# Performance work log

Measured on AMD Instinct MI355X. Metric: run time of the kernel, lower is better.

The kernel has to match this reference:

```python
import jax, jax.numpy as jnp
import numpy as np

B, E, H, DEPTH = 4096, 512, 512, 1
STRIDE = 2 * H * (DEPTH + 1)      # 2048
DEPTH_SIZE = 2 * 4 * H            # 4096


def setup_inputs() -> dict:
    key = jax.random.key(0)
    ks = jax.random.split(key, 12)
    s = 0.02
    return {
        "X": jax.random.normal(ks[0], (B, E), jnp.float32),
        "prev_a": jax.random.normal(ks[1], (B, DEPTH + 1, H), jnp.float32),
        "prev_b": jax.random.normal(ks[2], (B, DEPTH + 1, H), jnp.float32),
        "prev_depth": jax.random.randint(ks[3], (B, 1), 0, DEPTH + 1, jnp.int32),
        "Wa00": jax.random.normal(ks[4], (H, E + 2 * H), jnp.float32) * s,
        "Wa10": jax.random.normal(ks[5], (H, E + H), jnp.float32) * s,
        "Wb00": jax.random.normal(ks[6], (H, E + 2 * H), jnp.float32) * s,
        "Wb11": jax.random.normal(ks[7], (H, E + H), jnp.float32) * s,
        "Wb10": jax.random.normal(ks[8], (H, E + H), jnp.float32) * s,
        "Wb01": jax.random.normal(ks[9], (H, E + 2 * H), jnp.float32) * s,
        "Watt": jax.random.normal(ks[10], (4, DEPTH_SIZE * DEPTH), jnp.float32) * s,
    }


def reference(X, prev_a, prev_b, prev_depth, Wa00, Wa10, Wb00, Wb11, Wb10, Wb01, Watt):
    b = X.shape[0]
    pd = prev_depth.astype(X.dtype)  # [B,1], broadcasts over feature dim
    zeros2h = jnp.zeros((b, 2 * H), X.dtype)
    ab00, ab01, ab10, ab11 = [zeros2h], [zeros2h], [zeros2h], [zeros2h]
    for d in range(1, DEPTH + 1):
        fd = jnp.float32(d)
        a_d, a_dm1 = prev_a[:, d, :], prev_a[:, d - 1, :]
        b_d, b_dm1 = prev_b[:, d, :], prev_b[:, d - 1, :]
        # 'lt' branch multiplies zeros -> drop it; keep eq/gt terms only
        eq0, gt0 = (pd == fd).astype(X.dtype), (pd > fd).astype(X.dtype)
        eqp, gtp = (pd + 1 == fd).astype(X.dtype), (pd + 1 > fd).astype(X.dtype)
        eqm, gtm = (pd - 1 == fd).astype(X.dtype), (pd - 1 > fd).astype(X.dtype)
        fork_join_a = a_d
        nofork_nojoin_a = jnp.concatenate((X, b_dm1, a_d), 1) @ Wa00.T
        fork_nojoin_a = jnp.concatenate((X, b_dm1), 1) @ Wa10.T
        nofork_join_a = a_dm1
        na00 = eq0 * nofork_nojoin_a + gt0 * a_d
        na11 = eq0 * fork_join_a + gt0 * a_d
        na10 = eqp * fork_nojoin_a + gtp * a_d
        na01 = eqm * nofork_join_a + gtm * a_d
        fork_join_b = jnp.concatenate((X, b_d), 1) @ Wb11.T
        nofork_nojoin_b = jnp.concatenate((X, a_d, na00), 1) @ Wb00.T
        fork_nojoin_b = jnp.concatenate((X, na10), 1) @ Wb10.T
        nofork_join_b = jnp.concatenate((X, b_dm1, a_d), 1) @ Wb01.T
        nb00 = eq0 * nofork_nojoin_b + gt0 * b_d
        nb11 = eq0 * fork_join_b + gt0 * b_d
        nb10 = eqp * fork_nojoin_b + gtp * b_d
        nb01 = eqm * nofork_join_b + gtm * b_d
        ab00.append(jnp.concatenate((na00, nb00), 1))
        ab01.append(jnp.concatenate((na01, nb01), 1))
        ab10.append(jnp.concatenate((na10, nb10), 1))
        ab11.append(jnp.concatenate((na11, nb11), 1))
    # each branch: stack over depth+1 -> [B, stride]; concat branches -> [B, 4*stride]
    flats = [jnp.stack(lst, 1).reshape(b, -1) for lst in (ab00, ab01, ab10, ab11)]
    ns = jnp.concatenate(flats, 1)  # [B, 4*STRIDE]
    att = jax.nn.softmax(ns[:, DEPTH_SIZE:] @ Watt.T, axis=-1)  # [B,4]
    e0 = (pd == 0).astype(X.dtype)
    ed = (pd == DEPTH).astype(X.dtype)
    mask = jnp.concatenate((1 - e0, 1 - e0, 1 - ed, 1 - e0), 1)  # [B,4]
    att_vars = mask * att
    # np tiny underflows to 0 in fp32 -> selection is one-hot at the row max
    sel = jnp.sign(att_vars - att_vars.max(1, keepdims=True)) + 1.0
    # striper/stripe_expander bmm == per-row selection of one stride-block
    hidden = jnp.einsum('bc,bcs->bs', sel, ns.reshape(b, 4, STRIDE))
    hidden = hidden.reshape(b, DEPTH + 1, 2 * H)
    next_a = hidden[:, :, :H]
    next_b = hidden[:, :, H:]
    sel_i = sel.astype(prev_depth.dtype)
    pd0 = prev_depth[:, 0]
    next_depth = (sel_i[:, 0] * pd0 + sel_i[:, 1] * (pd0 - 1)
                  + sel_i[:, 2] * (pd0 + 1) + sel_i[:, 3] * pd0)[:, None]
    f = (sel[:, 2] + sel[:, 3])[:, None]
    j = (sel[:, 1] + sel[:, 3])[:, None]
    return next_a, next_b, next_depth, (f, j)
```

## Files before the change

### kernel.cpp

```cpp
#include <hip/hip_runtime.h>
#include <hip/hip_bf16.h>
#include <stdint.h>


typedef __attribute__((ext_vector_type(8))) short bf16x8;
typedef __attribute__((ext_vector_type(4))) float f32x4;

#define MB_ ((size_t)1 << 20)

static __device__ __forceinline__ unsigned short f2bf(float x) {
  unsigned u = __float_as_uint(x);
  return (unsigned short)((u + 0x7FFFu + ((u >> 16) & 1u)) >> 16);
}
static __device__ __forceinline__ float bf2f(unsigned short b) {
  return __uint_as_float((unsigned)b << 16);
}
static __device__ __forceinline__ void cvt8(float4 v0, float4 v1, uint4& hi, uint4& lo) {
  float v[8] = {v0.x, v0.y, v0.z, v0.w, v1.x, v1.y, v1.z, v1.w};
  unsigned hw[4], lw[4];
#pragma unroll
  for (int j = 0; j < 4; ++j) {
    unsigned short h0 = f2bf(v[2 * j]), h1 = f2bf(v[2 * j + 1]);
    unsigned short l0 = f2bf(v[2 * j] - bf2f(h0));
    unsigned short l1 = f2bf(v[2 * j + 1] - bf2f(h1));
    hw[j] = (unsigned)h0 | ((unsigned)h1 << 16);
    lw[j] = (unsigned)l0 | ((unsigned)l1 << 16);
  }
  hi = make_uint4(hw[0], hw[1], hw[2], hw[3]);
  lo = make_uint4(lw[0], lw[1], lw[2], lw[3]);
}

__global__ void kinit(float* nextA, float* nextB, int* cnt, int Bn) {
  long i = (long)blockIdx.x * blockDim.x + threadIdx.x;
  long st = (long)gridDim.x * blockDim.x;
  float4 z = make_float4(0.f, 0.f, 0.f, 0.f);
  long nA = (long)Bn * 128;
  for (long t = i; t < nA; t += st)
    ((float4*)(nextA + (t >> 7) * 1024))[t & 127] = z;
  long nB = (long)Bn * 256;
  for (long t = i; t < nB; t += st) ((float4*)nextB)[t] = z;
  if (blockIdx.x == 0 && threadIdx.x < 16) cnt[threadIdx.x] = 0;
}

struct CvtSeg { const float* src; unsigned short* dst; int srcStride; int gprow; long gbase; };
struct CvtArgs { CvtSeg s[5]; long total; };

__global__ void kcvt(CvtArgs a) {
  long g0 = (long)blockIdx.x * blockDim.x + threadIdx.x;
  long st = (long)gridDim.x * blockDim.x;
  for (long g = g0; g < a.total; g += st) {
    const float* src = a.s[0].src;
    unsigned short* dst = a.s[0].dst;
    int stride = a.s[0].srcStride, gp = a.s[0].gprow;
    long base = 0;
#pragma unroll
    for (int t = 1; t < 5; ++t) {
      if (g >= a.s[t].gbase) {
        src = a.s[t].src; dst = a.s[t].dst;
        stride = a.s[t].srcStride; gp = a.s[t].gprow; base = a.s[t].gbase;
      }
    }
    long lg = g - base;
    int row = (int)(lg / gp);
    int kp = (int)(lg - (long)row * gp);
    const float* p = src + (long)row * stride + kp * 8;
    uint4 hi, lo;
    cvt8(*(const float4*)p, *(const float4*)(p + 4), hi, lo);
    unsigned short* d = dst + (long)row * ((long)gp * 16) + (long)(kp >> 2) * 64 + (kp & 3) * 8;
    *(uint4*)d = hi;
    *(uint4*)(d + 32) = lo;
  }
}

__global__ void kclassify(const int* __restrict__ pdep, float* dep, float* fo, float* jo,
                          int* cnt, int* list0, int* list1, int Bn) {
  int r = blockIdx.x * blockDim.x + threadIdx.x;
  if (r >= Bn) return;
  if (pdep[r] == 0) {
    int p = atomicAdd(&cnt[0], 1);
    list0[p] = r;
    dep[r] = 1.0f; fo[r] = 1.0f; jo[r] = 0.0f;
  } else {
    int p = atomicAdd(&cnt[1], 1);
    list1[p] = r;
  }
}

struct GArgs {
  const float *X, *pa, *pb;
  float *nb11ws, *na00ws, *na10ws;
  const unsigned short *Wa10p, *Wb10p, *Wb11p, *Wa00p, *Wb00p;
  float *nextA, *nextB;
  const int *cnt, *list0, *list1, *list2, *list2i;
};

__global__ __launch_bounds__(256, 4) void gemm_mfma(GArgs G, int modeBase, int bpm) {
  int grp = (int)blockIdx.x / bpm;
  int bl = (int)blockIdx.x % bpm;
  int mode, ks;
  if (modeBase == 0) { mode = grp; ks = 0; }
  else { mode = modeBase; ks = grp; }
  int xcd = bl & 7, g = bl >> 3;
  int nt = g & 7, mt = (g >> 3) * 8 + xcd;

  const int* lst; int cntv, ktot;
  const unsigned short* W;
  if (mode == 0)      { lst = G.list0; cntv = G.cnt[0]; ktot = 32; W = G.Wa10p; }
  else if (mode == 1) { lst = G.list1; cntv = G.cnt[1]; ktot = 32; W = G.Wb11p; }
  else if (mode == 2) { lst = G.list1; cntv = G.cnt[1]; ktot = 48; W = G.Wa00p; }
  else if (mode == 3) { lst = G.list0; cntv = G.cnt[0]; ktot = 32; W = G.Wb10p; }
  else                { lst = G.list2; cntv = G.cnt[2]; ktot = 48; W = G.Wb00p; }
  if (mt * 64 >= cntv) return;
  const bool full3 = (mode == 1);
  const int kb0 = ks * 16;
  const int kb1 = (modeBase == 0) ? ktot : kb0 + 16;

  const int tid = threadIdx.x;
  const int arow = tid >> 2, kg = tid & 3;
  int mg = mt * 64 + arow;
  if (mg > cntv - 1) mg = cntv - 1;
  int r01 = lst[mg];
  const float* ab0 = G.X + (long)r01 * 512 + kg * 8;
  const float* ab1;
  const float* ab2 = nullptr;
  if (mode == 0)      ab1 = G.pb + (long)r01 * 1024 + kg * 8;
  else if (mode == 1) ab1 = G.pb + (long)r01 * 1024 + 512 + kg * 8;
  else if (mode == 2) {
    ab1 = G.pb + (long)r01 * 1024 + kg * 8;
    ab2 = G.pa + (long)r01 * 1024 + 512 + kg * 8;
  } else if (mode == 3) {
    ab1 = G.na10ws + (long)mg * 512 + kg * 8;
  } else {
    ab1 = G.pa + (long)r01 * 1024 + 512 + kg * 8;
    ab2 = G.na00ws + (long)G.list2i[mg] * 512 + kg * 8;
  }
  long wb = (long)(nt * 64 + arow) * (long)(ktot * 64) + kg * 8;

  __shared__ unsigned short lds[2][2][4096];

  float4 av0, av1;
  uint4 bhr, blr;
  auto gload = [&](int kb) {
    const float* p = (kb < 16) ? ab0 : (kb < 32) ? ab1 : ab2;
    p += (kb & 15) * 32;
    av0 = *(const float4*)p;
    av1 = *(const float4*)(p + 4);
    const unsigned short* q = W + wb + (long)kb * 64;
    bhr = *(const uint4*)q;
    blr = *(const uint4*)(q + 32);
  };
  auto lstore = [&](int b) {
    uint4 hi, lo;
    cvt8(av0, av1, hi, lo);
    *(uint4*)&lds[b][0][(kg * 64 + (arow ^ kg)) * 8] = hi;
    if (full3)
      *(uint4*)&lds[b][0][((kg + 4) * 64 + (arow ^ (kg + 4))) * 8] = lo;
    *(uint4*)&lds[b][1][(kg * 64 + (arow ^ kg)) * 8] = bhr;
    *(uint4*)&lds[b][1][((kg + 4) * 64 + (arow ^ (kg + 4))) * 8] = blr;
  };

  const int w = tid >> 6, lane = tid & 63;
  const int wrow = (w >> 1) * 32, wcol = (w & 1) * 32;
  const int gq = lane >> 4, lr = lane & 15;

  f32x4 acc[2][2];
#pragma unroll
  for (int i = 0; i < 2; ++i)
#pragma unroll
    for (int j = 0; j < 2; ++j) acc[i][j] = (f32x4){0.f, 0.f, 0.f, 0.f};

  gload(kb0);
  lstore(0);
  __syncthreads();
  int cur = 0;
  for (int kb = kb0; kb < kb1; ++kb) {
    if (kb + 1 < kb1) gload(kb + 1);
    bf16x8 ah[2], al[2], bh[2], bl[2];
#pragma unroll
    for (int t = 0; t < 2; ++t) {
      int rr = wrow + t * 16 + lr, cc = wcol + t * 16 + lr;
      ah[t] = *(const bf16x8*)&lds[cur][0][(gq * 64 + (rr ^ gq)) * 8];
      bh[t] = *(const bf16x8*)&lds[cur][1][(gq * 64 + (cc ^ gq)) * 8];
      bl[t] = *(const bf16x8*)&lds[cur][1][((gq + 4) * 64 + (cc ^ (gq + 4))) * 8];
      if (full3)
        al[t] = *(const bf16x8*)&lds[cur][0][((gq + 4) * 64 + (rr ^ (gq + 4))) * 8];
    }
#pragma unroll
    for (int rb = 0; rb < 2; ++rb)
#pragma unroll
      for (int cb = 0; cb < 2; ++cb) {
        acc[rb][cb] = __builtin_amdgcn_mfma_f32_16x16x32_bf16(ah[rb], bh[cb], acc[rb][cb], 0, 0, 0);
        acc[rb][cb] = __builtin_amdgcn_mfma_f32_16x16x32_bf16(ah[rb], bl[cb], acc[rb][cb], 0, 0, 0);
        if (full3)
          acc[rb][cb] = __builtin_amdgcn_mfma_f32_16x16x32_bf16(al[rb], bh[cb], acc[rb][cb], 0, 0, 0);
      }
    if (kb + 1 < kb1) lstore(cur ^ 1);
    __syncthreads();
    cur ^= 1;
  }

#pragma unroll
  for (int rb = 0; rb < 2; ++rb)
#pragma unroll
    for (int e = 0; e < 4; ++e) {
      int m = wrow + rb * 16 + (lane >> 4) * 4 + e;
      int mgo = mt * 64 + m;
      if (mgo >= cntv) continue;
#pragma unroll
      for (int cb = 0; cb < 2; ++cb) {
        int n = nt * 64 + wcol + cb * 16 + lr;
        float v = acc[rb][cb][e];
        if (mode == 0) {
          G.nextA[(long)G.list0[mgo] * 1024 + 512 + n] = v;
          G.na10ws[(long)mgo * 512 + n] = v;
        } else if (mode == 1) {
          G.nb11ws[(long)mgo * 512 + n] = v;
        } else if (mode == 2) {
          G.na00ws[(long)mgo * 512 + n] = v;
        } else {
          atomicAdd(G.nextB + (long)lst[mgo] * 1024 + 512 + n, v);
        }
      }
    }
}

__global__ __launch_bounds__(256) void kselect(
    const float* __restrict__ pa, const float* __restrict__ pb,
    const float* __restrict__ watt, const float* __restrict__ nb11ws,
    const float* __restrict__ na00ws,
    float* nextA, float* nextB, float* dep, float* fo, float* jo,
    int* cnt, const int* __restrict__ list1, int* list2, int* list2i) {
  int warp = threadIdx.x >> 6, lane = threadIdx.x & 63;
  int i1 = blockIdx.x * 4 + warp;
  if (i1 >= cnt[1]) return;
  int r = list1[i1];
  const float* a_d = pa + (long)r * 1024 + 512;
  const float* b_d = pb + (long)r * 1024 + 512;
  const float* nb = nb11ws + (long)i1 * 512;
  const float* na = na00ws + (long)i1 * 512;
  float av[8], nv[8];
  float z0 = 0.f, z1 = 0.f, z2 = 0.f, z3 = 0.f;
#pragma unroll
  for (int u = 0; u < 8; ++u) {
    int h = u * 64 + lane;
    float la = a_d[h], lb = b_d[h], ln = nb[h];
    av[u] = la; nv[u] = ln;
    z0 += (watt[1024 + h] + watt[3072 + h]) * la + watt[1536 + h] * lb + watt[3584 + h] * ln;
    z1 += (watt[5120 + h] + watt[7168 + h]) * la + watt[5632 + h] * lb + watt[7680 + h] * ln;
    z2 += (watt[9216 + h] + watt[11264 + h]) * la + watt[9728 + h] * lb + watt[11776 + h] * ln;
    z3 += (watt[13312 + h] + watt[15360 + h]) * la + watt[13824 + h] * lb + watt[15872 + h] * ln;
  }
#pragma unroll
  for (int off = 32; off; off >>= 1) {
    z0 += __shfl_xor(z0, off); z1 += __shfl_xor(z1, off);
    z2 += __shfl_xor(z2, off); z3 += __shfl_xor(z3, off);
  }
  float m = fmaxf(fmaxf(z0, z1), fmaxf(z2, z3));
  float e0 = expf(z0 - m), e1 = expf(z1 - m), e2 = expf(z2 - m), e3 = expf(z3 - m);
  float s = e0 + e1 + e2 + e3;
  float att0 = e0 / s, att1 = e1 / s, att3 = e3 / s;
  float amax = fmaxf(att0, fmaxf(att1, att3));
  float s0 = (att0 >= amax) ? 1.f : 0.f;
  float s1v = (att1 >= amax) ? 1.f : 0.f;
  float s3 = (att3 >= amax) ? 1.f : 0.f;
  if (lane == 0) {
    dep[r] = s0 + s3;
    fo[r] = s3;
    jo[r] = s1v + s3;
    if (s0 > 0.f) { int p = atomicAdd(&cnt[2], 1); list2[p] = r; list2i[p] = i1; }
  }
  float* dA = nextA + (long)r * 1024 + 512;
  float* dB = nextB + (long)r * 1024 + 512;
#pragma unroll
  for (int u = 0; u < 8; ++u) {
    int h = u * 64 + lane;
    float va = s3 * av[u];
    if (s0 > 0.f) va += na[h];
    dA[h] = va;
    dB[h] = s3 * nv[u];
  }
}

extern "C" void kernel_launch(void* const* d_in, const int* in_sizes, int n_in,
                              void* d_out, int out_size, void* d_ws, size_t ws_size,
                              hipStream_t stream) {
  const float* X = (const float*)d_in[0];
  const float* pa = (const float*)d_in[1];
  const float* pb = (const float*)d_in[2];
  const int* pdep = (const int*)d_in[3];
  const float* Wa00 = (const float*)d_in[4];
  const float* Wa10 = (const float*)d_in[5];
  const float* Wb00 = (const float*)d_in[6];
  const float* Wb11 = (const float*)d_in[7];
  const float* Wb10 = (const float*)d_in[8];
  const float* Watt = (const float*)d_in[10];
  const int Bn = in_sizes[3];

  float* out = (float*)d_out;
  float* nextA = out;
  float* nextB = out + (long)Bn * 1024;
  float* dep = out + (long)2 * Bn * 1024;
  float* fo = dep + Bn;
  float* jo = fo + Bn;

  char* ws = (char*)d_ws;
  int* cnt = (int*)ws;
  int* list0 = (int*)(ws + 1024);
  int* list1 = (int*)(ws + 1024 + 16384);
  int* list2 = (int*)(ws + 1024 + 2 * 16384);
  int* list2i = (int*)(ws + 1024 + 3 * 16384);
  float* nb11ws = (float*)(ws + 1 * MB_);
  float* na00ws = (float*)(ws + 9 * MB_);
  float* na10ws = (float*)(ws + 17 * MB_);
  unsigned short* Wa10p = (unsigned short*)(ws + 25 * MB_);
  unsigned short* Wb10p = (unsigned short*)(ws + 27 * MB_);
  unsigned short* Wb11p = (unsigned short*)(ws + 29 * MB_);
  unsigned short* Wa00p = (unsigned short*)(ws + 31 * MB_);
  unsigned short* Wb00p = (unsigned short*)(ws + 34 * MB_);

  kinit<<<1024, 256, 0, stream>>>(nextA, nextB, cnt, Bn);

  CvtArgs ca{};
  long gb = 0;
  auto seg = [&](int i, const float* s, unsigned short* d, int stride, int gprow, int rows) {
    ca.s[i].src = s; ca.s[i].dst = d; ca.s[i].srcStride = stride;
    ca.s[i].gprow = gprow; ca.s[i].gbase = gb;
    gb += (long)gprow * rows;
  };
  seg(0, Wa10, Wa10p, 1024, 128, 512);
  seg(1, Wb10, Wb10p, 1024, 128, 512);
  seg(2, Wb11, Wb11p, 1024, 128, 512);
  seg(3, Wa00, Wa00p, 1536, 192, 512);
  seg(4, Wb00, Wb00p, 1536, 192, 512);
  ca.total = gb;
  kcvt<<<512, 256, 0, stream>>>(ca);

  kclassify<<<(Bn + 255) / 256, 256, 0, stream>>>(pdep, dep, fo, jo, cnt, list0, list1, Bn);

  GArgs Ga;
  Ga.X = X; Ga.pa = pa; Ga.pb = pb;
  Ga.nb11ws = nb11ws; Ga.na00ws = na00ws; Ga.na10ws = na10ws;
  Ga.Wa10p = Wa10p; Ga.Wb10p = Wb10p; Ga.Wb11p = Wb11p;
  Ga.Wa00p = Wa00p; Ga.Wb00p = Wb00p;
  Ga.nextA = nextA; Ga.nextB = nextB;
  Ga.cnt = cnt; Ga.list0 = list0; Ga.list1 = list1; Ga.list2 = list2; Ga.list2i = list2i;

  int nmb = (Bn + 63) / 64;
  int nm8 = ((nmb + 7) / 8) * 8;
  int bpm = nm8 * 8;

  gemm_mfma<<<3 * bpm, 256, 0, stream>>>(Ga, 0, bpm);
  kselect<<<(Bn + 3) / 4, 256, 0, stream>>>(pa, pb, Watt, nb11ws, na00ws, nextA, nextB,
                                            dep, fo, jo, cnt, list1, list2, list2i);
  gemm_mfma<<<2 * bpm, 256, 0, stream>>>(Ga, 3, bpm);
  gemm_mfma<<<3 * bpm, 256, 0, stream>>>(Ga, 4, bpm);
}
```

Measured before the change: 236.9 us.

## Fuse init, weight-convert and classify kernels; deepen GEMM global-load prefetch

Merges the zero-init, weight bf16 split conversion and row classification kernels into a single launch partitioned by block index, and replaces the counter reset with a memset. In the MFMA GEMM, global loads are now issued two k-steps ahead using two register stage sets, so that LDS stores and compute overlap with more outstanding memory traffic. This cuts launch overhead and hides load latency, at the cost of more registers per thread, which may lower occupancy under the launch bound.

```diff
diff --git a/kernel.cpp b/kernel.cpp
--- a/kernel.cpp
+++ b/kernel.cpp
@@ -30,59 +30,59 @@
   lo = make_uint4(lw[0], lw[1], lw[2], lw[3]);
 }
 
-__global__ void kinit(float* nextA, float* nextB, int* cnt, int Bn) {
-  long i = (long)blockIdx.x * blockDim.x + threadIdx.x;
-  long st = (long)gridDim.x * blockDim.x;
-  float4 z = make_float4(0.f, 0.f, 0.f, 0.f);
-  long nA = (long)Bn * 128;
-  for (long t = i; t < nA; t += st)
-    ((float4*)(nextA + (t >> 7) * 1024))[t & 127] = z;
-  long nB = (long)Bn * 256;
-  for (long t = i; t < nB; t += st) ((float4*)nextB)[t] = z;
-  if (blockIdx.x == 0 && threadIdx.x < 16) cnt[threadIdx.x] = 0;
-}
-
 struct CvtSeg { const float* src; unsigned short* dst; int srcStride; int gprow; long gbase; };
 struct CvtArgs { CvtSeg s[5]; long total; };
 
-__global__ void kcvt(CvtArgs a) {
-  long g0 = (long)blockIdx.x * blockDim.x + threadIdx.x;
-  long st = (long)gridDim.x * blockDim.x;
-  for (long g = g0; g < a.total; g += st) {
-    const float* src = a.s[0].src;
-    unsigned short* dst = a.s[0].dst;
-    int stride = a.s[0].srcStride, gp = a.s[0].gprow;
-    long base = 0;
-#pragma unroll
-    for (int t = 1; t < 5; ++t) {
-      if (g >= a.s[t].gbase) {
-        src = a.s[t].src; dst = a.s[t].dst;
-        stride = a.s[t].srcStride; gp = a.s[t].gprow; base = a.s[t].gbase;
+__global__ __launch_bounds__(256) void kprep(float* nextA, float* nextB, CvtArgs a,
+                                             const int* __restrict__ pdep, float* dep,
+                                             float* fo, float* jo, int* cnt,
+                                             int* list0, int* list1, int Bn) {
+  int b = blockIdx.x, tid = threadIdx.x;
+  if (b < 512) {
+    long i = (long)b * 256 + tid;
+    const long st = 512 * 256;
+    float4 z = make_float4(0.f, 0.f, 0.f, 0.f);
+    long nA = (long)Bn * 128;
+    for (long t = i; t < nA; t += st)
+      ((float4*)(nextA + (t >> 7) * 1024))[t & 127] = z;
+    long nB = (long)Bn * 256;
+    for (long t = i; t < nB; t += st) ((float4*)nextB)[t] = z;
+  } else if (b < 1024) {
+    long g0 = (long)(b - 512) * 256 + tid;
+    const long st = 512 * 256;
+    for (long g = g0; g < a.total; g += st) {
+      const float* src = a.s[0].src;
+      unsigned short* dst = a.s[0].dst;
+      int stride = a.s[0].srcStride, gp = a.s[0].gprow;
+      long base = 0;
+#pragma unroll
+      for (int t = 1; t < 5; ++t) {
+        if (g >= a.s[t].gbase) {
+          src = a.s[t].src; dst = a.s[t].dst;
+          stride = a.s[t].srcStride; gp = a.s[t].gprow; base = a.s[t].gbase;
+        }
       }
+      long lg = g - base;
+      int row = (int)(lg / gp);
+      int kp = (int)(lg - (long)row * gp);
+      const float* p = src + (long)row * stride + kp * 8;
+      uint4 hi, lo;
+      cvt8(*(const float4*)p, *(const float4*)(p + 4), hi, lo);
+      unsigned short* d = dst + (long)row * ((long)gp * 16) + (long)(kp >> 2) * 64 + (kp & 3) * 8;
+      *(uint4*)d = hi;
+      *(uint4*)(d + 32) = lo;
     }
-    long lg = g - base;
-    int row = (int)(lg / gp);
-    int kp = (int)(lg - (long)row * gp);
-    const float* p = src + (long)row * stride + kp * 8;
-    uint4 hi, lo;
-    cvt8(*(const float4*)p, *(const float4*)(p + 4), hi, lo);
-    unsigned short* d = dst + (long)row * ((long)gp * 16) + (long)(kp >> 2) * 64 + (kp & 3) * 8;
-    *(uint4*)d = hi;
-    *(uint4*)(d + 32) = lo;
-  }
-}
-
-__global__ void kclassify(const int* __restrict__ pdep, float* dep, float* fo, float* jo,
-                          int* cnt, int* list0, int* list1, int Bn) {
-  int r = blockIdx.x * blockDim.x + threadIdx.x;
-  if (r >= Bn) return;
-  if (pdep[r] == 0) {
-    int p = atomicAdd(&cnt[0], 1);
-    list0[p] = r;
-    dep[r] = 1.0f; fo[r] = 1.0f; jo[r] = 0.0f;
   } else {
-    int p = atomicAdd(&cnt[1], 1);
-    list1[p] = r;
+    int r = (b - 1024) * 256 + tid;
+    if (r >= Bn) return;
+    if (pdep[r] == 0) {
+      int p = atomicAdd(&cnt[0], 1);
+      list0[p] = r;
+      dep[r] = 1.0f; fo[r] = 1.0f; jo[r] = 0.0f;
+    } else {
+      int p = atomicAdd(&cnt[1], 1);
+      list1[p] = r;
+    }
   }
 }
 
@@ -138,25 +138,23 @@
 
   __shared__ unsigned short lds[2][2][4096];
 
-  float4 av0, av1;
-  uint4 bhr, blr;
-  auto gload = [&](int kb) {
+  auto gload = [&](int kb, float4& v0, float4& v1, uint4& bh_, uint4& bl_) {
     const float* p = (kb < 16) ? ab0 : (kb < 32) ? ab1 : ab2;
     p += (kb & 15) * 32;
-    av0 = *(const float4*)p;
-    av1 = *(const float4*)(p + 4);
+    v0 = *(const float4*)p;
+    v1 = *(const float4*)(p + 4);
     const unsigned short* q = W + wb + (long)kb * 64;
-    bhr = *(const uint4*)q;
-    blr = *(const uint4*)(q + 32);
+    bh_ = *(const uint4*)q;
+    bl_ = *(const uint4*)(q + 32);
   };
-  auto lstore = [&](int b) {
+  auto lstore = [&](int b, float4 v0, float4 v1, uint4 bh_, uint4 bl_) {
     uint4 hi, lo;
-    cvt8(av0, av1, hi, lo);
+    cvt8(v0, v1, hi, lo);
     *(uint4*)&lds[b][0][(kg * 64 + (arow ^ kg)) * 8] = hi;
     if (full3)
       *(uint4*)&lds[b][0][((kg + 4) * 64 + (arow ^ (kg + 4))) * 8] = lo;
-    *(uint4*)&lds[b][1][(kg * 64 + (arow ^ kg)) * 8] = bhr;
-    *(uint4*)&lds[b][1][((kg + 4) * 64 + (arow ^ (kg + 4))) * 8] = blr;
+    *(uint4*)&lds[b][1][(kg * 64 + (arow ^ kg)) * 8] = bh_;
+    *(uint4*)&lds[b][1][((kg + 4) * 64 + (arow ^ (kg + 4))) * 8] = bl_;
   };
 
   const int w = tid >> 6, lane = tid & 63;
@@ -169,21 +167,16 @@
 #pragma unroll
     for (int j = 0; j < 2; ++j) acc[i][j] = (f32x4){0.f, 0.f, 0.f, 0.f};
 
-  gload(kb0);
-  lstore(0);
-  __syncthreads();
-  int cur = 0;
-  for (int kb = kb0; kb < kb1; ++kb) {
-    if (kb + 1 < kb1) gload(kb + 1);
+  auto compute = [&](int b) {
     bf16x8 ah[2], al[2], bh[2], bl[2];
 #pragma unroll
     for (int t = 0; t < 2; ++t) {
       int rr = wrow + t * 16 + lr, cc = wcol + t * 16 + lr;
-      ah[t] = *(const bf16x8*)&lds[cur][0][(gq * 64 + (rr ^ gq)) * 8];
-      bh[t] = *(const bf16x8*)&lds[cur][1][(gq * 64 + (cc ^ gq)) * 8];
-      bl[t] = *(const bf16x8*)&lds[cur][1][((gq + 4) * 64 + (cc ^ (gq + 4))) * 8];
+      ah[t] = *(const bf16x8*)&lds[b][0][(gq * 64 + (rr ^ gq)) * 8];
+      bh[t] = *(const bf16x8*)&lds[b][1][(gq * 64 + (cc ^ gq)) * 8];
+      bl[t] = *(const bf16x8*)&lds[b][1][((gq + 4) * 64 + (cc ^ (gq + 4))) * 8];
       if (full3)
-        al[t] = *(const bf16x8*)&lds[cur][0][((gq + 4) * 64 + (rr ^ (gq + 4))) * 8];
+        al[t] = *(const bf16x8*)&lds[b][0][((gq + 4) * 64 + (rr ^ (gq + 4))) * 8];
     }
 #pragma unroll
     for (int rb = 0; rb < 2; ++rb)
@@ -194,7 +187,25 @@
         if (full3)
           acc[rb][cb] = __builtin_amdgcn_mfma_f32_16x16x32_bf16(al[rb], bh[cb], acc[rb][cb], 0, 0, 0);
       }
-    if (kb + 1 < kb1) lstore(cur ^ 1);
+  };
+
+  float4 s0a0, s0a1, s1a0, s1a1;
+  uint4 s0bh, s0bl, s1bh, s1bl;
+  gload(kb0, s0a0, s0a1, s0bh, s0bl);
+  if (kb0 + 1 < kb1) gload(kb0 + 1, s1a0, s1a1, s1bh, s1bl);
+  lstore(0, s0a0, s0a1, s0bh, s0bl);
+  __syncthreads();
+  int cur = 0;
+  for (int kb = kb0; kb < kb1; kb += 2) {
+    if (kb + 2 < kb1) gload(kb + 2, s0a0, s0a1, s0bh, s0bl);
+    if (kb + 1 < kb1) lstore(cur ^ 1, s1a0, s1a1, s1bh, s1bl);
+    compute(cur);
+    __syncthreads();
+    cur ^= 1;
+    if (kb + 1 >= kb1) break;
+    if (kb + 3 < kb1) gload(kb + 3, s1a0, s1a1, s1bh, s1bl);
+    if (kb + 2 < kb1) lstore(cur ^ 1, s0a0, s0a1, s0bh, s0bl);
+    compute(cur);
     __syncthreads();
     cur ^= 1;
   }
@@ -318,7 +329,7 @@
   unsigned short* Wa00p = (unsigned short*)(ws + 31 * MB_);
   unsigned short* Wb00p = (unsigned short*)(ws + 34 * MB_);
 
-  kinit<<<1024, 256, 0, stream>>>(nextA, nextB, cnt, Bn);
+  hipMemsetAsync(cnt, 0, 64, stream);
 
   CvtArgs ca{};
   long gb = 0;
@@ -333,9 +344,10 @@
   seg(3, Wa00, Wa00p, 1536, 192, 512);
   seg(4, Wb00, Wb00p, 1536, 192, 512);
   ca.total = gb;
-  kcvt<<<512, 256, 0, stream>>>(ca);
-
-  kclassify<<<(Bn + 255) / 256, 256, 0, stream>>>(pdep, dep, fo, jo, cnt, list0, list1, Bn);
+
+  int clsBlocks = (Bn + 255) / 256;
+  kprep<<<1024 + clsBlocks, 256, 0, stream>>>(nextA, nextB, ca, pdep, dep, fo, jo,
+                                              cnt, list0, list1, Bn);
 
   GArgs Ga;
   Ga.X = X; Ga.pa = pa; Ga.pb = pb;
```

New measurement: 226.4 us. 4.4% less time.
